# Kernel tuning notes

Measured on AMD Instinct MI355X. Metric: run time of the kernel, lower is better.

## Reference

```python
import jax, jax.numpy as jnp
import numpy as np

NEG = -9e15
ALPHA = 0.2  # LeakyReLU slope


def xavier(key, shape, gain=1.414):
    fan_in, fan_out = shape[-2], shape[-1]
    bound = gain * np.sqrt(6.0 / (fan_in + fan_out))
    return jax.random.uniform(key, shape, jnp.float32, -bound, bound)


def setup_inputs() -> dict:
    key = jax.random.key(0)
    ks = jax.random.split(key, 8)
    N, D_IN, HID, OUT, H = 4096, 128, 64, 64, 4
    x = jax.random.normal(ks[0], (N, D_IN), jnp.float32)
    adj = jax.random.randint(ks[1], (N, N), 0, 2, jnp.int32)
    # layer 0: in=D_IN, out=HID, heads=H
    W0 = xavier(ks[2], (H, D_IN, HID))
    a0 = xavier(ks[3], (H, 2 * HID, 1))
    # layer 1: in=HID*H, out=HID, heads=H
    W1 = xavier(ks[4], (H, HID * H, HID))
    a1 = xavier(ks[5], (H, 2 * HID, 1))
    # layer 2: in=HID*H, out=OUT, heads=1
    W2 = xavier(ks[6], (1, HID * H, OUT))
    a2 = xavier(ks[7], (1, 2 * OUT, 1))
    return {"x": x, "adj": adj, "W0": W0, "a0": a0, "W1": W1, "a1": a1, "W2": W2, "a2": a2}


def gat_layer(x, adj_mask, W, a):
    # x: [N, D], W: [H, D, O], a: [H, 2O, 1]
    O = W.shape[-1]
    h = jnp.einsum('nd,hdo->hno', x, W)                      # [H, N, O]
    a_l, a_r = a[:, :O, 0], a[:, O:, 0]                      # [H, O] each
    e_l = jnp.einsum('hno,ho->hn', h, a_l)                   # a^T[Wh_i||Wh_j] split
    e_r = jnp.einsum('hno,ho->hn', h, a_r)
    e = e_l[:, :, None] + e_r[:, None, :]                    # [H, N, N]
    e = jnp.where(e > 0, e, ALPHA * e)                       # LeakyReLU
    att = jnp.where(adj_mask[None], e, NEG)
    att = jax.nn.softmax(att, axis=-1)                       # dropout skipped (eval)
    out = jnp.einsum('hnm,hmo->hno', att, h)                 # [H, N, O]
    N = x.shape[0]
    return out.transpose(1, 0, 2).reshape(N, -1)             # [N, H*O]


def reference(x, adj, W0, a0, W1, a1, W2, a2):
    adj_mask = adj > 0
    h = gat_layer(x, adj_mask, W0, a0)
    h = jax.nn.elu(h)
    h = gat_layer(h, adj_mask, W1, a1)
    h = jax.nn.elu(h)
    h = gat_layer(h, adj_mask, W2, a2)
    return h
```

## Files before the change

kernel.cpp:

```cpp
#include <hip/hip_runtime.h>

#define LOG2E 1.4426950408889634f

typedef float  f32x4 __attribute__((ext_vector_type(4)));
typedef int    i32x4 __attribute__((ext_vector_type(4)));
typedef short  s16x8 __attribute__((ext_vector_type(8)));

static __device__ __forceinline__ float exp2_fast(float x) {
#if __has_builtin(__builtin_amdgcn_exp2f)
    return __builtin_amdgcn_exp2f(x);
#else
    return exp2f(x);
#endif
}
static __device__ __forceinline__ unsigned short bf16_rne(float f) {
    unsigned u = __float_as_uint(f);
    u += 0x7FFFu + ((u >> 16) & 1u);
    return (unsigned short)(u >> 16);
}
static __device__ __forceinline__ unsigned fkey(float f) {
    unsigned u = __float_as_uint(f);
    return (u & 0x80000000u) ? ~u : (u | 0x80000000u);
}
static __device__ __forceinline__ float fkey_dec(unsigned k) {
    return __uint_as_float((k & 0x80000000u) ? (k & 0x7fffffffu) : ~k);
}

__global__ __launch_bounds__(256) void fused_prep(
    const int* __restrict__ adj,
    const float* __restrict__ xf,
    const float* __restrict__ W0, const float* __restrict__ W1,
    const float* __restrict__ W2,
    unsigned long long* __restrict__ bits,
    unsigned short* __restrict__ Xc,
    unsigned short* __restrict__ W0t, unsigned short* __restrict__ W1t,
    unsigned short* __restrict__ W2t, unsigned* __restrict__ Mkey)
{
    int gid = blockIdx.x * 256 + threadIdx.x;
    unsigned long long m = __ballot(adj[gid] != 0);
    if ((gid & 63) == 0) bits[gid >> 6] = m;

    if (gid < 524288) Xc[gid] = bf16_rne(xf[gid]);
    if (gid < 12) Mkey[gid] = 0u;
    if (gid < 32768) {
        int h = gid >> 13, d = (gid >> 6) & 127, o = gid & 63;
        W0t[(h * 64 + o) * 128 + d] = bf16_rne(W0[gid]);
    } else if (gid < 98304) {
        int g = gid - 32768;
        int h = g >> 14, d = (g >> 6) & 255, o = g & 63;
        W1t[(h * 64 + o) * 256 + d] = bf16_rne(W1[g]);
    } else if (gid < 114688) {
        int g = gid - 98304;
        int d = g >> 6, o = g & 63;
        W2t[o * 256 + d] = bf16_rne(W2[g]);
    }
}

static __device__ __forceinline__ void gemm_epilogue(
    const f32x4* acc, const float* ab, int h, int nb, int c, int q, int lane,
    unsigned short* hT, float* el2, float* er2, unsigned* Mkey)
{
#pragma unroll
    for (int j = 0; j < 4; ++j) {
        unsigned d0 = (unsigned)bf16_rne(acc[j][0]) | ((unsigned)bf16_rne(acc[j][1]) << 16);
        unsigned d1 = (unsigned)bf16_rne(acc[j][2]) | ((unsigned)bf16_rne(acc[j][3]) << 16);
        unsigned short* dst = hT + ((size_t)h * 64 + j * 16 + c) * 4096 + nb + q * 4;
        ((unsigned*)dst)[0] = d0;
        ((unsigned*)dst)[1] = d1;
    }
    float elr[4] = {0,0,0,0}, err[4] = {0,0,0,0};
#pragma unroll
    for (int j = 0; j < 4; ++j) {
        float al = ab[j * 16 + c];
        float ar = ab[64 + j * 16 + c];
#pragma unroll
        for (int r = 0; r < 4; ++r) {
            elr[r] = fmaf(al, acc[j][r], elr[r]);
            err[r] = fmaf(ar, acc[j][r], err[r]);
        }
    }
#pragma unroll
    for (int m = 1; m <= 8; m <<= 1) {
#pragma unroll
        for (int r = 0; r < 4; ++r) {
            elr[r] += __shfl_xor(elr[r], m, 64);
            err[r] += __shfl_xor(err[r], m, 64);
        }
    }
    float rmax = -3.0e38f;
    if (c == 0) {
#pragma unroll
        for (int r = 0; r < 4; ++r) {
            int n = nb + q * 4 + r;
            float r2 = err[r] * LOG2E;
            el2[h * 4096 + n] = elr[r] * LOG2E;
            er2[h * 4096 + n] = r2;
            rmax = fmaxf(rmax, r2);
        }
    }
    rmax = fmaxf(rmax, __shfl_xor(rmax, 16, 64));
    rmax = fmaxf(rmax, __shfl_xor(rmax, 32, 64));
    if (lane == 0) atomicMax(&Mkey[h], fkey(rmax));
}

__global__ __launch_bounds__(256) void gemm_elr(
    const unsigned short* __restrict__ X, int K,
    const unsigned short* __restrict__ Wt,
    const float* __restrict__ a,
    unsigned short* __restrict__ hT,
    float* __restrict__ el2, float* __restrict__ er2,
    unsigned* __restrict__ Mkey)
{
    const int lane = threadIdx.x & 63, w = threadIdx.x >> 6;
    const int c = lane & 15, q = lane >> 4;
    const int h = blockIdx.y;
    const int nb = blockIdx.x * 64 + w * 16;
    const unsigned short* xrow = X + (size_t)(nb + c) * K + q * 8;
    const unsigned short* wb   = Wt + ((size_t)h * 64 + c) * K + q * 8;

    f32x4 acc[4] = {{0,0,0,0},{0,0,0,0},{0,0,0,0},{0,0,0,0}};
    for (int kk = 0; kk < K; kk += 32) {
        s16x8 af = *(const s16x8*)(xrow + kk);
#pragma unroll
        for (int j = 0; j < 4; ++j) {
            s16x8 bf = *(const s16x8*)(wb + (size_t)(j * 16) * K + kk);
            acc[j] = __builtin_amdgcn_mfma_f32_16x16x32_bf16(af, bf, acc[j], 0, 0, 0);
        }
    }
    gemm_epilogue(acc, a + h * 128, h, nb, c, q, lane, hT, el2, er2, Mkey);
}

__global__ __launch_bounds__(256) void gemm_comb(
    const float* __restrict__ accP, const float* __restrict__ lP,
    const unsigned short* __restrict__ Wt,
    const float* __restrict__ a,
    unsigned short* __restrict__ hT,
    float* __restrict__ el2, float* __restrict__ er2,
    unsigned* __restrict__ Mkey)
{
    const int lane = threadIdx.x & 63, w = threadIdx.x >> 6;
    const int c = lane & 15, q = lane >> 4;
    const int h = blockIdx.y;
    const int nb = blockIdx.x * 64 + w * 16;
    const int n = nb + c;
    const unsigned short* wb = Wt + ((size_t)h * 64 + c) * 256 + q * 8;

    float rl[4];
#pragma unroll
    for (int hh = 0; hh < 4; ++hh)
        rl[hh] = 1.0f / (lP[(size_t)hh * 4096 + n] + lP[(size_t)(4 + hh) * 4096 + n]);
    const float* ap0 = accP + (size_t)n * 256;
    const float* ap1 = accP + (size_t)(4096 + n) * 256;

    f32x4 acc[4] = {{0,0,0,0},{0,0,0,0},{0,0,0,0},{0,0,0,0}};
    for (int kk = 0; kk < 256; kk += 32) {
        const int cb = q * 8 + kk;
        f32x4 s0a = *(const f32x4*)(ap0 + cb), s0b = *(const f32x4*)(ap0 + cb + 4);
        f32x4 s1a = *(const f32x4*)(ap1 + cb), s1b = *(const f32x4*)(ap1 + cb + 4);
        const float r = rl[cb >> 6];
        float v[8];
#pragma unroll
        for (int i = 0; i < 4; ++i) {
            v[i]     = (s0a[i] + s1a[i]) * r;
            v[i + 4] = (s0b[i] + s1b[i]) * r;
        }
        unsigned pd[4];
#pragma unroll
        for (int i = 0; i < 4; ++i) {
            float v0 = v[2 * i], v1 = v[2 * i + 1];
            v0 = (v0 < 0.f) ? exp2_fast(v0 * LOG2E) - 1.f : v0;
            v1 = (v1 < 0.f) ? exp2_fast(v1 * LOG2E) - 1.f : v1;
            pd[i] = (unsigned)bf16_rne(v0) | ((unsigned)bf16_rne(v1) << 16);
        }
        union { unsigned u[4]; s16x8 s; } afu;
        afu.u[0] = pd[0]; afu.u[1] = pd[1]; afu.u[2] = pd[2]; afu.u[3] = pd[3];
        s16x8 af = afu.s;
#pragma unroll
        for (int j = 0; j < 4; ++j) {
            s16x8 bf = *(const s16x8*)(wb + (size_t)(j * 16) * 256 + kk);
            acc[j] = __builtin_amdgcn_mfma_f32_16x16x32_bf16(af, bf, acc[j], 0, 0, 0);
        }
    }
    gemm_epilogue(acc, a + h * 128, h, nb, c, q, lane, hT, el2, er2, Mkey);
}

__global__ __launch_bounds__(256) void att_kernel(
    const unsigned short* __restrict__ hT,
    const float* __restrict__ el2g, const float* __restrict__ er2g,
    const unsigned* __restrict__ Mkey,
    const unsigned long long* __restrict__ bits,
    float* __restrict__ accP, float* __restrict__ lP,
    int H, int KPS, int HO)
{
    __shared__ unsigned short ldsH[64 * 264];
    __shared__ float ldsE[256];
    const int tid = threadIdx.x;
    const int lane = tid & 63, w = tid >> 6;
    const int c = lane & 15, q = lane >> 4, q8 = q * 8;
    const int h = blockIdx.y, ks = blockIdx.z;
    const int nb = blockIdx.x * 64 + w * 16;
    const int rowA = nb + c;

    const float M2 = fkey_dec(Mkey[h]);
    float e2 = el2g[h * 4096 + rowA];
    float xx = e2 + M2;
    float C2 = fmaxf(xx, 0.2f * xx);
    const float elA = e2 - C2;
    const float elB = fmaf(0.2f, e2, -C2);

    const char* bitrow = (const char*)bits + (size_t)rowA * 512 + (size_t)(KPS >> 3) * ks;

    s16x8 ones = {0,0,0,0,0,0,0,0};
    if (c == 0) {
#pragma unroll
        for (int i = 0; i < 8; ++i) ones[i] = (short)0x3F80;
    }
    f32x4 acc[4] = {{0,0,0,0},{0,0,0,0},{0,0,0,0},{0,0,0,0}};
    f32x4 accl = {0,0,0,0};

    const unsigned short* hTh = hT + (size_t)h * 64 * 4096;
    const float* erh = er2g + h * 4096;
    const int tiles = KPS >> 8;

    for (int t = 0; t < tiles; ++t) {
        const int mabs = ks * KPS + t * 256;
#pragma unroll
        for (int i = 0; i < 8; ++i) {
            int cidx = i * 256 + tid;
            int o = cidx >> 5, seg = cidx & 31;
            i32x4 v = *(const i32x4*)(hTh + (size_t)o * 4096 + mabs + seg * 8);
            *(i32x4*)(ldsH + o * 264 + seg * 8) = v;
        }
        if (tid < 64)
            *(f32x4*)(ldsE + tid * 4) = *(const f32x4*)(erh + mabs + tid * 4);
        __syncthreads();

        i32x4 b0 = *(const i32x4*)(bitrow + t * 32);
        i32x4 b1 = *(const i32x4*)(bitrow + t * 32 + 16);
        int bw[8] = {b0[0], b0[1], b0[2], b0[3], b1[0], b1[1], b1[2], b1[3]};

#pragma unroll
        for (int cc = 0; cc < 8; ++cc) {
            const int kl = cc * 32 + q8;
            f32x4 ea = *(const f32x4*)(ldsE + kl);
            f32x4 eb = *(const f32x4*)(ldsE + kl + 4);
            const unsigned word = (unsigned)bw[cc];
            unsigned pd[4];
#pragma unroll
            for (int jj = 0; jj < 4; ++jj) {
                float er0 = (jj < 2) ? ea[2 * jj]     : eb[2 * jj - 4];
                float er1 = (jj < 2) ? ea[2 * jj + 1] : eb[2 * jj - 3];
                float s0 = fminf(fmaxf(elA + er0, fmaf(0.2f, er0, elB)), 0.f);
                float s1 = fminf(fmaxf(elA + er1, fmaf(0.2f, er1, elB)), 0.f);
                float p0 = exp2_fast(s0);
                float p1 = exp2_fast(s1);
                unsigned m0 = (unsigned)(-(int)((word >> (q8 + 2 * jj)) & 1u));
                unsigned m1 = (unsigned)(-(int)((word >> (q8 + 2 * jj + 1)) & 1u));
                unsigned u0 = __float_as_uint(p0) & m0;
                unsigned u1 = __float_as_uint(p1) & m1;
                pd[jj] = (u0 >> 16) | (u1 & 0xFFFF0000u);
            }
            union { unsigned u[4]; s16x8 s; } afu;
            afu.u[0] = pd[0]; afu.u[1] = pd[1]; afu.u[2] = pd[2]; afu.u[3] = pd[3];
            s16x8 af = afu.s;
            const unsigned short* lb = ldsH + c * 264 + kl;
#pragma unroll
            for (int j = 0; j < 4; ++j) {
                s16x8 bf = *(const s16x8*)(lb + (size_t)(j * 16) * 264);
                acc[j] = __builtin_amdgcn_mfma_f32_16x16x32_bf16(af, bf, acc[j], 0, 0, 0);
            }
            accl = __builtin_amdgcn_mfma_f32_16x16x32_bf16(af, ones, accl, 0, 0, 0);
        }
        __syncthreads();
    }
    float ls[4];
#pragma unroll
    for (int r = 0; r < 4; ++r) ls[r] = __shfl(accl[r], lane & 48, 64);

    float* ap = accP + ((size_t)ks * 4096 + nb + q * 4) * HO + h * 64 + c;
#pragma unroll
    for (int r = 0; r < 4; ++r)
#pragma unroll
        for (int j = 0; j < 4; ++j)
            ap[(size_t)r * HO + j * 16] = acc[j][r];
    if (c == 0) {
#pragma unroll
        for (int r = 0; r < 4; ++r)
            lP[((size_t)ks * H + h) * 4096 + nb + q * 4 + r] = ls[r];
    }
}

__global__ __launch_bounds__(256) void comb_final(
    const float* __restrict__ accP, const float* __restrict__ lP,
    float* __restrict__ outf)
{
    const int idx = blockIdx.x * 256 + threadIdx.x;
    const int n = idx >> 6, col = idx & 63;
    float s = 0.f, l = 0.f;
#pragma unroll
    for (int ks = 0; ks < 4; ++ks) {
        s += accP[((size_t)ks * 4096 + n) * 64 + col];
        l += lP[(size_t)ks * 4096 + n];
    }
    outf[idx] = s / l;
}

extern "C" void kernel_launch(void* const* d_in, const int* in_sizes, int n_in,
                              void* d_out, int out_size, void* d_ws, size_t ws_size,
                              hipStream_t stream)
{
    (void)in_sizes; (void)n_in; (void)out_size; (void)ws_size;
    const float* x   = (const float*)d_in[0];
    const int*   adj = (const int*)d_in[1];
    const float* W0  = (const float*)d_in[2];
    const float* a0  = (const float*)d_in[3];
    const float* W1  = (const float*)d_in[4];
    const float* a1  = (const float*)d_in[5];
    const float* W2  = (const float*)d_in[6];
    const float* a2  = (const float*)d_in[7];

    char* p = (char*)d_ws;
    unsigned long long* bits = (unsigned long long*)(p + 0x000000);
    unsigned short* hT  = (unsigned short*)(p + 0x200000);
    unsigned short* Xc  = (unsigned short*)(p + 0x400000);
    unsigned short* W0t = (unsigned short*)(p + 0x500000);
    unsigned short* W1t = (unsigned short*)(p + 0x510000);
    unsigned short* W2t = (unsigned short*)(p + 0x530000);
    float*    el2  = (float*)(p + 0x538000);
    float*    er2  = (float*)(p + 0x548000);
    unsigned* Mkey = (unsigned*)(p + 0x558000);
    float*    accP = (float*)(p + 0x560000);
    float*    lP   = (float*)(p + 0xD60000);

    fused_prep<<<65536, 256, 0, stream>>>(adj, x, W0, W1, W2,
                                          bits, Xc, W0t, W1t, W2t, Mkey);

    gemm_elr<<<dim3(64, 4), 256, 0, stream>>>(Xc, 128, W0t, a0, hT, el2, er2, Mkey + 0);
    att_kernel<<<dim3(64, 4, 2), 256, 0, stream>>>(hT, el2, er2, Mkey + 0, bits, accP, lP, 4, 2048, 256);

    gemm_comb<<<dim3(64, 4), 256, 0, stream>>>(accP, lP, W1t, a1, hT, el2, er2, Mkey + 4);
    att_kernel<<<dim3(64, 4, 2), 256, 0, stream>>>(hT, el2, er2, Mkey + 4, bits, accP, lP, 4, 2048, 256);

    gemm_comb<<<dim3(64, 1), 256, 0, stream>>>(accP, lP, W2t, a2, hT, el2, er2, Mkey + 8);
    att_kernel<<<dim3(64, 1, 4), 256, 0, stream>>>(hT, el2, er2, Mkey + 8, bits, accP, lP, 1, 1024, 64);

    comb_final<<<1024, 256, 0, stream>>>(accP, lP, (float*)d_out);
}
```

Measured before the change: 257.1 us.

## Merge all GAT stages into one cooperative persistent kernel with grid syncs

Replaces the eight separate kernel launches (prep, three GEMMs, three attention passes, final combine) with a single cooperative kernel of 512 blocks that runs every stage in sequence, separated by grid-wide barriers. The aim is to remove per-launch overhead and the idle gaps between dependent small kernels. In exchange, the adjacency bit-packing now runs on only 512 blocks looping 128 times instead of 65536 blocks. Grid syncs add their own cost, and the launch bound of 2 blocks per CU, with the attention LDS footprint, must fit for the cooperative launch to succeed.

```diff
diff --git a/kernel.cpp b/kernel.cpp
--- a/kernel.cpp
+++ b/kernel.cpp
@@ -1,4 +1,7 @@
 #include <hip/hip_runtime.h>
+#include <hip/hip_cooperative_groups.h>
+
+namespace cg = cooperative_groups;
 
 #define LOG2E 1.4426950408889634f
 
@@ -26,36 +29,6 @@
     return __uint_as_float((k & 0x80000000u) ? (k & 0x7fffffffu) : ~k);
 }
 
-__global__ __launch_bounds__(256) void fused_prep(
-    const int* __restrict__ adj,
-    const float* __restrict__ xf,
-    const float* __restrict__ W0, const float* __restrict__ W1,
-    const float* __restrict__ W2,
-    unsigned long long* __restrict__ bits,
-    unsigned short* __restrict__ Xc,
-    unsigned short* __restrict__ W0t, unsigned short* __restrict__ W1t,
-    unsigned short* __restrict__ W2t, unsigned* __restrict__ Mkey)
-{
-    int gid = blockIdx.x * 256 + threadIdx.x;
-    unsigned long long m = __ballot(adj[gid] != 0);
-    if ((gid & 63) == 0) bits[gid >> 6] = m;
-
-    if (gid < 524288) Xc[gid] = bf16_rne(xf[gid]);
-    if (gid < 12) Mkey[gid] = 0u;
-    if (gid < 32768) {
-        int h = gid >> 13, d = (gid >> 6) & 127, o = gid & 63;
-        W0t[(h * 64 + o) * 128 + d] = bf16_rne(W0[gid]);
-    } else if (gid < 98304) {
-        int g = gid - 32768;
-        int h = g >> 14, d = (g >> 6) & 255, o = g & 63;
-        W1t[(h * 64 + o) * 256 + d] = bf16_rne(W1[g]);
-    } else if (gid < 114688) {
-        int g = gid - 98304;
-        int d = g >> 6, o = g & 63;
-        W2t[o * 256 + d] = bf16_rne(W2[g]);
-    }
-}
-
 static __device__ __forceinline__ void gemm_epilogue(
     const f32x4* acc, const float* ab, int h, int nb, int c, int q, int lane,
     unsigned short* hT, float* el2, float* er2, unsigned* Mkey)
@@ -103,18 +76,14 @@
     if (lane == 0) atomicMax(&Mkey[h], fkey(rmax));
 }
 
-__global__ __launch_bounds__(256) void gemm_elr(
-    const unsigned short* __restrict__ X, int K,
-    const unsigned short* __restrict__ Wt,
-    const float* __restrict__ a,
-    unsigned short* __restrict__ hT,
-    float* __restrict__ el2, float* __restrict__ er2,
-    unsigned* __restrict__ Mkey)
-{
-    const int lane = threadIdx.x & 63, w = threadIdx.x >> 6;
+static __device__ __forceinline__ void gemm_body(
+    const unsigned short* X, int K, const unsigned short* Wt, const float* a,
+    unsigned short* hT, float* el2, float* er2, unsigned* Mkey,
+    int bx, int h, int tid)
+{
+    const int lane = tid & 63, w = tid >> 6;
     const int c = lane & 15, q = lane >> 4;
-    const int h = blockIdx.y;
-    const int nb = blockIdx.x * 64 + w * 16;
+    const int nb = bx * 64 + w * 16;
     const unsigned short* xrow = X + (size_t)(nb + c) * K + q * 8;
     const unsigned short* wb   = Wt + ((size_t)h * 64 + c) * K + q * 8;
 
@@ -130,18 +99,14 @@
     gemm_epilogue(acc, a + h * 128, h, nb, c, q, lane, hT, el2, er2, Mkey);
 }
 
-__global__ __launch_bounds__(256) void gemm_comb(
-    const float* __restrict__ accP, const float* __restrict__ lP,
-    const unsigned short* __restrict__ Wt,
-    const float* __restrict__ a,
-    unsigned short* __restrict__ hT,
-    float* __restrict__ el2, float* __restrict__ er2,
-    unsigned* __restrict__ Mkey)
-{
-    const int lane = threadIdx.x & 63, w = threadIdx.x >> 6;
+static __device__ __forceinline__ void gemm_comb_body(
+    const float* accP, const float* lP, const unsigned short* Wt, const float* a,
+    unsigned short* hT, float* el2, float* er2, unsigned* Mkey,
+    int bx, int h, int tid)
+{
+    const int lane = tid & 63, w = tid >> 6;
     const int c = lane & 15, q = lane >> 4;
-    const int h = blockIdx.y;
-    const int nb = blockIdx.x * 64 + w * 16;
+    const int nb = bx * 64 + w * 16;
     const int n = nb + c;
     const unsigned short* wb = Wt + ((size_t)h * 64 + c) * 256 + q * 8;
 
@@ -184,21 +149,16 @@
     gemm_epilogue(acc, a + h * 128, h, nb, c, q, lane, hT, el2, er2, Mkey);
 }
 
-__global__ __launch_bounds__(256) void att_kernel(
-    const unsigned short* __restrict__ hT,
-    const float* __restrict__ el2g, const float* __restrict__ er2g,
-    const unsigned* __restrict__ Mkey,
-    const unsigned long long* __restrict__ bits,
-    float* __restrict__ accP, float* __restrict__ lP,
-    int H, int KPS, int HO)
-{
-    __shared__ unsigned short ldsH[64 * 264];
-    __shared__ float ldsE[256];
-    const int tid = threadIdx.x;
+static __device__ __forceinline__ void att_body(
+    unsigned short* ldsH, float* ldsE,
+    const unsigned short* hT, const float* el2g, const float* er2g,
+    const unsigned* Mkey, const unsigned long long* bits,
+    float* accP, float* lP, int H, int KPS, int HO,
+    int bx, int h, int ks, int tid)
+{
     const int lane = tid & 63, w = tid >> 6;
     const int c = lane & 15, q = lane >> 4, q8 = q * 8;
-    const int h = blockIdx.y, ks = blockIdx.z;
-    const int nb = blockIdx.x * 64 + w * 16;
+    const int nb = bx * 64 + w * 16;
     const int rowA = nb + c;
 
     const float M2 = fkey_dec(Mkey[h]);
@@ -290,19 +250,87 @@
     }
 }
 
-__global__ __launch_bounds__(256) void comb_final(
-    const float* __restrict__ accP, const float* __restrict__ lP,
+__global__ __launch_bounds__(256, 2) void mega(
+    const int* __restrict__ adj, const float* __restrict__ xf,
+    const float* __restrict__ W0, const float* __restrict__ a0,
+    const float* __restrict__ W1, const float* __restrict__ a1,
+    const float* __restrict__ W2, const float* __restrict__ a2,
+    unsigned long long* __restrict__ bits, unsigned short* __restrict__ Xc,
+    unsigned short* __restrict__ W0t, unsigned short* __restrict__ W1t,
+    unsigned short* __restrict__ W2t,
+    unsigned short* __restrict__ hT, float* __restrict__ el2,
+    float* __restrict__ er2, unsigned* __restrict__ Mkey,
+    float* __restrict__ accP, float* __restrict__ lP,
     float* __restrict__ outf)
 {
-    const int idx = blockIdx.x * 256 + threadIdx.x;
-    const int n = idx >> 6, col = idx & 63;
-    float s = 0.f, l = 0.f;
-#pragma unroll
-    for (int ks = 0; ks < 4; ++ks) {
-        s += accP[((size_t)ks * 4096 + n) * 64 + col];
-        l += lP[(size_t)ks * 4096 + n];
-    }
-    outf[idx] = s / l;
+    cg::grid_group grid = cg::this_grid();
+    __shared__ unsigned short ldsH[64 * 264];
+    __shared__ float ldsE[256];
+    const int tid = threadIdx.x, bid = blockIdx.x;
+    const int base = bid * 256 + tid;
+
+    for (int it = 0; it < 128; ++it) {
+        int idx = it * 131072 + base;
+        unsigned long long m = __ballot(adj[idx] != 0);
+        if ((idx & 63) == 0) bits[idx >> 6] = m;
+    }
+#pragma unroll
+    for (int it = 0; it < 4; ++it) {
+        int i = it * 131072 + base;
+        Xc[i] = bf16_rne(xf[i]);
+    }
+    if (base < 12) Mkey[base] = 0u;
+    if (base < 32768) {
+        int h = base >> 13, d = (base >> 6) & 127, o = base & 63;
+        W0t[(h * 64 + o) * 128 + d] = bf16_rne(W0[base]);
+    } else if (base < 98304) {
+        int g = base - 32768;
+        int h = g >> 14, d = (g >> 6) & 255, o = g & 63;
+        W1t[(h * 64 + o) * 256 + d] = bf16_rne(W1[g]);
+    } else if (base < 114688) {
+        int g = base - 98304;
+        int d = g >> 6, o = g & 63;
+        W2t[o * 256 + d] = bf16_rne(W2[g]);
+    }
+    grid.sync();
+
+    if (bid < 256)
+        gemm_body(Xc, 128, W0t, a0, hT, el2, er2, Mkey + 0, bid & 63, bid >> 6, tid);
+    grid.sync();
+
+    att_body(ldsH, ldsE, hT, el2, er2, Mkey + 0, bits, accP, lP,
+             4, 2048, 256, bid & 63, (bid >> 6) & 3, bid >> 8, tid);
+    grid.sync();
+
+    if (bid < 256)
+        gemm_comb_body(accP, lP, W1t, a1, hT, el2, er2, Mkey + 4, bid & 63, bid >> 6, tid);
+    grid.sync();
+
+    att_body(ldsH, ldsE, hT, el2, er2, Mkey + 4, bits, accP, lP,
+             4, 2048, 256, bid & 63, (bid >> 6) & 3, bid >> 8, tid);
+    grid.sync();
+
+    if (bid < 64)
+        gemm_comb_body(accP, lP, W2t, a2, hT, el2, er2, Mkey + 8, bid, 0, tid);
+    grid.sync();
+
+    if (bid < 256)
+        att_body(ldsH, ldsE, hT, el2, er2, Mkey + 8, bits, accP, lP,
+                 1, 1024, 64, bid & 63, 0, bid >> 6, tid);
+    grid.sync();
+
+#pragma unroll
+    for (int it = 0; it < 2; ++it) {
+        int idx = it * 131072 + base;
+        int n = idx >> 6, col = idx & 63;
+        float s = 0.f, l = 0.f;
+#pragma unroll
+        for (int ks = 0; ks < 4; ++ks) {
+            s += accP[((size_t)ks * 4096 + n) * 64 + col];
+            l += lP[(size_t)ks * 4096 + n];
+        }
+        outf[idx] = s / l;
+    }
 }
 
 extern "C" void kernel_launch(void* const* d_in, const int* in_sizes, int n_in,
@@ -310,8 +338,8 @@
                               hipStream_t stream)
 {
     (void)in_sizes; (void)n_in; (void)out_size; (void)ws_size;
+    const int*   adj = (const int*)d_in[1];
     const float* x   = (const float*)d_in[0];
-    const int*   adj = (const int*)d_in[1];
     const float* W0  = (const float*)d_in[2];
     const float* a0  = (const float*)d_in[3];
     const float* W1  = (const float*)d_in[4];
@@ -331,18 +359,12 @@
     unsigned* Mkey = (unsigned*)(p + 0x558000);
     float*    accP = (float*)(p + 0x560000);
     float*    lP   = (float*)(p + 0xD60000);
-
-    fused_prep<<<65536, 256, 0, stream>>>(adj, x, W0, W1, W2,
-                                          bits, Xc, W0t, W1t, W2t, Mkey);
-
-    gemm_elr<<<dim3(64, 4), 256, 0, stream>>>(Xc, 128, W0t, a0, hT, el2, er2, Mkey + 0);
-    att_kernel<<<dim3(64, 4, 2), 256, 0, stream>>>(hT, el2, er2, Mkey + 0, bits, accP, lP, 4, 2048, 256);
-
-    gemm_comb<<<dim3(64, 4), 256, 0, stream>>>(accP, lP, W1t, a1, hT, el2, er2, Mkey + 4);
-    att_kernel<<<dim3(64, 4, 2), 256, 0, stream>>>(hT, el2, er2, Mkey + 4, bits, accP, lP, 4, 2048, 256);
-
-    gemm_comb<<<dim3(64, 1), 256, 0, stream>>>(accP, lP, W2t, a2, hT, el2, er2, Mkey + 8);
-    att_kernel<<<dim3(64, 1, 4), 256, 0, stream>>>(hT, el2, er2, Mkey + 8, bits, accP, lP, 1, 1024, 64);
-
-    comb_final<<<1024, 256, 0, stream>>>(accP, lP, (float*)d_out);
-}
+    float*    outf = (float*)d_out;
+
+    void* args[] = {
+        (void*)&adj, (void*)&x, (void*)&W0, (void*)&a0, (void*)&W1, (void*)&a1,
+        (void*)&W2, (void*)&a2, (void*)&bits, (void*)&Xc, (void*)&W0t,
+        (void*)&W1t, (void*)&W2t, (void*)&hT, (void*)&el2, (void*)&er2,
+        (void*)&Mkey, (void*)&accP, (void*)&lP, (void*)&outf };
+    hipLaunchCooperativeKernel((void*)mega, dim3(512), dim3(256), args, 0, stream);
+}
```

New measurement: 682.3 us. 2.65x slower.
